# Optimization experiments

Measured on AMD Instinct MI355X. Metric: run time of the kernel, lower is better.

## Reference

```python
import jax, jax.numpy as jnp
import numpy as np

N = 100000
E = 1600000
D_IN, H1, H2 = 64, 128, 64
ATT = 32


def _mean_aggregate(feat, src, dst, num_nodes):
    # gather source features per edge, scatter-sum to destinations, divide by in-degree
    summed = jax.ops.segment_sum(feat[src], dst, num_segments=num_nodes)  # [N, d]
    deg = jax.ops.segment_sum(jnp.ones((src.shape[0],), feat.dtype), dst, num_segments=num_nodes)
    return summed / jnp.maximum(deg, 1.0)[:, None]


def setup_inputs() -> dict:
    key = jax.random.key(0)
    ks = jax.random.split(key, 16)
    x = jax.random.normal(ks[0], (N, D_IN), dtype=jnp.float32)
    edge_index = jax.random.randint(ks[1], (2, E), 0, N, dtype=jnp.int64)

    def lin(k, fan_in, fan_out):
        bound = 1.0 / np.sqrt(fan_in)
        return jax.random.uniform(k, (fan_in, fan_out), jnp.float32, -bound, bound)

    params = {
        'W1_l': lin(ks[2], D_IN, H1), 'W1_r': lin(ks[3], D_IN, H1),
        'b1': jnp.zeros((H1,), jnp.float32),
        'W2_l': lin(ks[4], H1, H2), 'W2_r': lin(ks[5], H1, H2),
        'b2': jnp.zeros((H2,), jnp.float32),
        'Wa': lin(ks[6], H2, ATT), 'ba': jnp.zeros((ATT,), jnp.float32),
        'ctx': jax.random.normal(ks[7], (ATT,), jnp.float32),
        'Wc1': lin(ks[8], H2, H2 // 2), 'bc1': jnp.zeros((H2 // 2,), jnp.float32),
        'Wc2': lin(ks[9], H2 // 2, 1), 'bc2': jnp.zeros((1,), jnp.float32),
    }
    return {'x': x, 'edge_index': edge_index, **params}


def reference(x, edge_index, W1_l, W1_r, b1, W2_l, W2_r, b2, Wa, ba, ctx, Wc1, bc1, Wc2, bc2):
    src, dst = edge_index[0], edge_index[1]
    ionm_alerts = x[:, -1]  # [N]

    # GraphSAGE layer 1 (mean aggr): lin_l(mean_neighbors) + lin_r(x_self)
    agg1 = _mean_aggregate(x, src, dst, N)
    h = jax.nn.relu(agg1 @ W1_l + b1 + x @ W1_r)  # [N, H1]
    # F.dropout(training=False) -> identity

    # GraphSAGE layer 2
    agg2 = _mean_aggregate(h, src, dst, N)
    h = jax.nn.relu(agg2 @ W2_l + b2 + h @ W2_r)  # [N, H2]

    # attention with IONM alert boost (+0.4)
    scores = jnp.tanh(h @ Wa + ba)            # [N, ATT]
    w = scores @ ctx + ionm_alerts * 0.4       # [N]
    w = jax.nn.softmax(w, axis=0)
    h = h * w[:, None]

    pooled = jnp.mean(h, axis=0, keepdims=True)  # [1, H2]

    # classifier head (Dropout identity in eval)
    z = jax.nn.relu(pooled @ Wc1 + bc1)
    return jax.nn.sigmoid(z @ Wc2 + bc2)  # [1, 1]
```

## Files before the change

kernel.cpp:

```cpp
#include <hip/hip_runtime.h>
#include <math.h>

#define N_NODES 100000
#define E_EDGES 1600000
#define D_IN 64
#define HID1 128
#define HID2 64
#define ATT 32
#define CAP 64
#define AT_STRIDE 136
#define NRANGE 4
#define RNODES (N_NODES / NRANGE)
#define NPART 64
#define XCAST_BLOCKS ((N_NODES * 16 + 255) / 256)
#define SCAT_BLOCKS 1024

typedef unsigned int uint32;
typedef unsigned short ushort;
typedef __attribute__((ext_vector_type(8))) short short8;
typedef __attribute__((ext_vector_type(4))) float float4v;

#define NTL(p) __builtin_nontemporal_load(&(p))

__device__ inline uint32 bf16rn(float f){ uint32 u = __float_as_uint(f); return (u + 0x7fffu + ((u >> 16) & 1u)) >> 16; }
__device__ inline uint32 packbf2(float a, float b){ return bf16rn(a) | (bf16rn(b) << 16); }

#if __has_builtin(__builtin_amdgcn_cvt_f32_fp8) && __has_builtin(__builtin_amdgcn_cvt_pk_fp8_f32)
#define HW_FP8 1
#endif

__device__ inline uint32 fp8_enc_sw(float f){
    float a = fabsf(f);
    uint32 s = (__float_as_uint(f) >> 24) & 0x80u;
    if (!(a >= 0.001953125f)) return s;
    if (a > 448.f) return s | 0x7Eu;
    if (a < 0.015625f){
        uint32 c = (uint32)rintf(a * 512.f);
        return s | c;
    }
    int e; float m = frexpf(a, &e);
    int E = e - 1;
    float mant = 2.f * m;
    uint32 mc = (uint32)rintf((mant - 1.f) * 8.f);
    uint32 Ec = (uint32)(E + 7);
    if (mc == 8u){ mc = 0u; Ec += 1u; }
    if (Ec >= 16u || (Ec == 15u && mc > 6u)) return s | 0x7Eu;
    return s | (Ec << 3) | mc;
}

__device__ inline float fp8_dec_sw(uint32 c){
    uint32 s = (c & 0x80u) << 24;
    uint32 E = (c >> 3) & 0xFu, m = c & 7u;
    float v;
    if (E == 0) v = (float)m * 0.001953125f;
    else v = __uint_as_float(((E + 120u) << 23) | (m << 20));
    return __uint_as_float(__float_as_uint(v) | s);
}

__device__ inline uint32 enc4(float a, float b, float c, float d){
#ifdef HW_FP8
    int r = __builtin_amdgcn_cvt_pk_fp8_f32(a, b, 0, false);
    r = __builtin_amdgcn_cvt_pk_fp8_f32(c, d, r, true);
    return (uint32)r;
#else
    return fp8_enc_sw(a) | (fp8_enc_sw(b) << 8) | (fp8_enc_sw(c) << 16) | (fp8_enc_sw(d) << 24);
#endif
}

__device__ inline void dec4acc(uint32 w, float& a0, float& a1, float& a2, float& a3){
#ifdef HW_FP8
    a0 += __builtin_amdgcn_cvt_f32_fp8((int)w, 0);
    a1 += __builtin_amdgcn_cvt_f32_fp8((int)w, 1);
    a2 += __builtin_amdgcn_cvt_f32_fp8((int)w, 2);
    a3 += __builtin_amdgcn_cvt_f32_fp8((int)w, 3);
#else
    a0 += fp8_dec_sw(w & 0xffu);
    a1 += fp8_dec_sw((w >> 8) & 0xffu);
    a2 += fp8_dec_sw((w >> 16) & 0xffu);
    a3 += fp8_dec_sw(w >> 24);
#endif
}

__global__ void k_mega(const float* __restrict__ x,
                       const int* __restrict__ src, const int* __restrict__ dst,
                       const float* __restrict__ W1l, const float* __restrict__ W1r,
                       const float* __restrict__ W2l, const float* __restrict__ W2r,
                       uint32* __restrict__ xb, uint32* __restrict__ xq,
                       uint32* __restrict__ vq,
                       ushort* __restrict__ wt1g, ushort* __restrict__ wt2g,
                       int* __restrict__ cnt, int* __restrict__ ssrc){
    int b = blockIdx.x, t = threadIdx.x;
    if (b < XCAST_BLOCKS){
        int i = b * 256 + t;
        if (i < N_NODES * 16){
            float4v v = NTL(((const float4v*)x)[i]);
            xb[2 * i]     = packbf2(v.x, v.y);
            xb[2 * i + 1] = packbf2(v.z, v.w);
            xq[i] = enc4(v.x, v.y, v.z, v.w);
        }
        return;
    }
    if (b < XCAST_BLOCKS + 2){
        int sub = b - XCAST_BLOCKS;
        ushort* dstp = (sub == 0) ? wt1g : wt2g;
        for (int idx = t; idx < 128 * 128; idx += 256){
            int nn = idx >> 7, kk = idx & 127;
            float v;
            if (sub == 0) v = (kk < 64) ? W1l[kk * 128 + nn] : W1r[(kk - 64) * 128 + nn];
            else          v = (nn < 64) ? W2l[kk * 64 + nn]  : W2r[kk * 64 + (nn - 64)];
            dstp[nn * 128 + kk] = (ushort)bf16rn(v);
        }
        if (sub == 0){
            if (t < 16) xq[(size_t)N_NODES * 16 + t] = 0u;
            else if (t < 32) vq[(size_t)N_NODES * 16 + (t - 16)] = 0u;
        }
        return;
    }
    int rel = b - (XCAST_BLOCKS + 2);
    int range = rel & (NRANGE - 1);
    int blk   = rel >> 2;
    int lo = range * RNODES, hi = lo + RNODES;
    int stride = (SCAT_BLOCKS >> 2) * 256;
    for (int i = blk * 256 + t; i < E_EDGES; i += stride){
        int d = NTL(dst[i]);
        if (d >= lo && d < hi){
            int pos = atomicAdd(&cnt[d], 1);
            if (pos < CAP) ssrc[d * CAP + pos] = NTL(src[i]);
        }
    }
}

__device__ inline void gather8_fp8(const uint32* __restrict__ tab,
                                   const int* __restrict__ ssrc,
                                   const int* __restrict__ cnt,
                                   int n0, int lane,
                                   float acc[8][4], int cct[8]){
    int q = lane >> 4, p = lane & 15;
    int nn = n0 + (lane & 7);
    int ccl_ = cnt[nn];
    int cc[8];
    #pragma unroll
    for (int j = 0; j < 8; j++){
        int c = __shfl(ccl_, j, 64);
        cct[j] = c;
        cc[j] = min(c, CAP);
    }
    #pragma unroll
    for (int j = 0; j < 8; j++){ acc[j][0] = acc[j][1] = acc[j][2] = acc[j][3] = 0.f; }
    int cmax = 0;
    #pragma unroll
    for (int j = 0; j < 8; j++) cmax = max(cmax, cc[j]);
    if (cmax == 0) return;
    int se[8];
    #pragma unroll
    for (int j = 0; j < 8; j++){
        se[j] = (lane < cc[j]) ? NTL(ssrc[(n0 + j) * CAP + lane]) : N_NODES;
    }
    int iters = (cmax + 3) >> 2;
    uint32 w[8];
    #pragma unroll
    for (int j = 0; j < 8; j++){
        int s = __shfl(se[j], q, 64);
        w[j] = tab[(uint32)s * 16u + p];
    }
    for (int it = 0; it < iters; it++){
        uint32 wn[8];
        bool more = (it + 1 < iters);
        int idxn = (it + 1) * 4 + q;
        if (more){
            #pragma unroll
            for (int j = 0; j < 8; j++){
                int s = __shfl(se[j], idxn, 64);
                wn[j] = tab[(uint32)s * 16u + p];
            }
        }
        #pragma unroll
        for (int j = 0; j < 8; j++)
            dec4acc(w[j], acc[j][0], acc[j][1], acc[j][2], acc[j][3]);
        if (more){
            #pragma unroll
            for (int j = 0; j < 8; j++) w[j] = wn[j];
        }
    }
    #pragma unroll
    for (int j = 0; j < 8; j++){
        acc[j][0] += __shfl_xor(acc[j][0], 16, 64); acc[j][1] += __shfl_xor(acc[j][1], 16, 64);
        acc[j][2] += __shfl_xor(acc[j][2], 16, 64); acc[j][3] += __shfl_xor(acc[j][3], 16, 64);
        acc[j][0] += __shfl_xor(acc[j][0], 32, 64); acc[j][1] += __shfl_xor(acc[j][1], 32, 64);
        acc[j][2] += __shfl_xor(acc[j][2], 32, 64); acc[j][3] += __shfl_xor(acc[j][3], 32, 64);
    }
}

__global__ __launch_bounds__(256) void k_layer1(
    const uint32* __restrict__ xq, const uint32* __restrict__ xb,
    const int* __restrict__ ssrc, const int* __restrict__ cnt,
    const ushort* __restrict__ wt1g, const ushort* __restrict__ wt2g,
    const float* __restrict__ b1, const float* __restrict__ b2,
    uint32* __restrict__ vq, float* __restrict__ r2f){
    __shared__ ushort smem[2 * 32 * AT_STRIDE];
    ushort* at  = smem;
    ushort* at2 = smem + 32 * AT_STRIDE;
    float* vstage = (float*)smem;
    int t = threadIdx.x, wave = t >> 6, lane = t & 63;
    int nb0 = blockIdx.x * 32;
    int n0 = nb0 + wave * 8;

    int m0 = t >> 3, ch = t & 7;
    uint4 xval = *(const uint4*)&xb[(size_t)(nb0 + m0) * 32 + ch * 4];

    float acc[8][4]; int cct[8];
    gather8_fp8(xq, ssrc, cnt, n0, lane, acc, cct);
    int p = lane & 15;
    if (lane < 16){
        #pragma unroll
        for (int j = 0; j < 8; j++){
            float inv = 1.f / fmaxf((float)cct[j], 1.f);
            uint2 o;
            o.x = packbf2(acc[j][0] * inv, acc[j][1] * inv);
            o.y = packbf2(acc[j][2] * inv, acc[j][3] * inv);
            *(uint2*)&at[(wave * 8 + j) * AT_STRIDE + 4 * p] = o;
        }
    }
    *(uint4*)((uint32*)(at + m0 * AT_STRIDE + 64) + ch * 4) = xval;
    __syncthreads();

    int cidx = lane & 15, quad = lane >> 4;
    int mt = wave >> 1;
    int nbase = (wave & 1) * 64;
    float4v c[4];
    #pragma unroll
    for (int nt = 0; nt < 4; nt++) c[nt] = (float4v){0.f,0.f,0.f,0.f};
    #pragma unroll
    for (int kt = 0; kt < 4; kt++){
        short8 a = *(short8*)(at + ((mt * 16 + cidx) * AT_STRIDE + kt * 32 + quad * 8));
        #pragma unroll
        for (int nt = 0; nt < 4; nt++){
            short8 b = *(const short8*)(wt1g + ((nbase + nt * 16 + cidx) * 128 + kt * 32 + quad * 8));
            c[nt] = __builtin_amdgcn_mfma_f32_16x16x32_bf16(a, b, c[nt], 0, 0, 0);
        }
    }
    #pragma unroll
    for (int nt = 0; nt < 4; nt++){
        float bb = b1[nbase + nt * 16 + cidx];
        #pragma unroll
        for (int i = 0; i < 4; i++){
            int row = quad * 4 + i;
            at2[(mt * 16 + row) * AT_STRIDE + nbase + nt * 16 + cidx] =
                (ushort)bf16rn(fmaxf(c[nt][i] + bb, 0.f));
        }
    }
    __syncthreads();
    #pragma unroll
    for (int nt = 0; nt < 4; nt++) c[nt] = (float4v){0.f,0.f,0.f,0.f};
    #pragma unroll
    for (int kt = 0; kt < 4; kt++){
        short8 a = *(short8*)(at2 + ((mt * 16 + cidx) * AT_STRIDE + kt * 32 + quad * 8));
        #pragma unroll
        for (int nt = 0; nt < 4; nt++){
            short8 b = *(const short8*)(wt2g + ((nbase + nt * 16 + cidx) * 128 + kt * 32 + quad * 8));
            c[nt] = __builtin_amdgcn_mfma_f32_16x16x32_bf16(a, b, c[nt], 0, 0, 0);
        }
    }
    if (nbase == 0){
        #pragma unroll
        for (int nt = 0; nt < 4; nt++){
            #pragma unroll
            for (int i = 0; i < 4; i++){
                int row = quad * 4 + i;
                vstage[(mt * 16 + row) * 65 + nt * 16 + cidx] = c[nt][i];
            }
        }
    } else {
        #pragma unroll
        for (int nt = 0; nt < 4; nt++){
            float bb = b2[nt * 16 + cidx];
            #pragma unroll
            for (int i = 0; i < 4; i++){
                int row = quad * 4 + i;
                size_t node = nb0 + mt * 16 + row;
                r2f[node * 64 + nt * 16 + cidx] = c[nt][i] + bb;
            }
        }
    }
    __syncthreads();
    {
        int m = t >> 3, u = t & 7;
        float f0 = vstage[m * 65 + 8 * u],     f1 = vstage[m * 65 + 8 * u + 1];
        float f2 = vstage[m * 65 + 8 * u + 2], f3 = vstage[m * 65 + 8 * u + 3];
        float f4 = vstage[m * 65 + 8 * u + 4], f5 = vstage[m * 65 + 8 * u + 5];
        float f6 = vstage[m * 65 + 8 * u + 6], f7 = vstage[m * 65 + 8 * u + 7];
        vq[(size_t)(nb0 + m) * 16 + 2 * u]     = enc4(f0, f1, f2, f3);
        vq[(size_t)(nb0 + m) * 16 + 2 * u + 1] = enc4(f4, f5, f6, f7);
    }
}

__global__ __launch_bounds__(256) void k_gather2f(
    const float* __restrict__ x, const uint32* __restrict__ vq,
    const int* __restrict__ ssrc, const int* __restrict__ cnt,
    const float* __restrict__ r2f,
    const float* __restrict__ Wa, const float* __restrict__ ba, const float* __restrict__ ctx,
    float* __restrict__ pooledP, float* __restrict__ Zpart){
    __shared__ float sh2[32][68];
    __shared__ float sew[32];
    __shared__ float sp[4][64];
    int t = threadIdx.x, wave = t >> 6, lane = t & 63;
    int bn0 = blockIdx.x * 32;
    int n0 = bn0 + wave * 8;
    float acc[8][4]; int cct[8];
    gather8_fp8(vq, ssrc, cnt, n0, lane, acc, cct);
    int p = lane & 15;
    if (lane < 16){
        #pragma unroll
        for (int j = 0; j < 8; j++){
            size_t nj = n0 + j;
            float inv = 1.f / fmaxf((float)cct[j], 1.f);
            float4v rr = NTL(*(const float4v*)&r2f[nj * 64 + 4 * p]);
            float4v hv;
            hv.x = fmaxf(acc[j][0] * inv + rr.x, 0.f);
            hv.y = fmaxf(acc[j][1] * inv + rr.y, 0.f);
            hv.z = fmaxf(acc[j][2] * inv + rr.z, 0.f);
            hv.w = fmaxf(acc[j][3] * inv + rr.w, 0.f);
            *(float4v*)&sh2[wave * 8 + j][4 * p] = hv;
        }
    }
    __syncthreads();
    int node = t >> 3;
    int c0 = (t & 7) * 4;
    float s0 = ba[c0], s1 = ba[c0 + 1], s2 = ba[c0 + 2], s3 = ba[c0 + 3];
    #pragma unroll 8
    for (int j = 0; j < 64; j++){
        float hv = sh2[node][j];
        s0 += hv * Wa[j * ATT + c0];
        s1 += hv * Wa[j * ATT + c0 + 1];
        s2 += hv * Wa[j * ATT + c0 + 2];
        s3 += hv * Wa[j * ATT + c0 + 3];
    }
    float pa = tanhf(s0) * ctx[c0] + tanhf(s1) * ctx[c0 + 1]
             + tanhf(s2) * ctx[c0 + 2] + tanhf(s3) * ctx[c0 + 3];
    #pragma unroll
    for (int off = 4; off >= 1; off >>= 1) pa += __shfl_down(pa, off, 8);
    if ((t & 7) == 0){
        int n = bn0 + node;
        float w = pa + NTL(x[(size_t)n * 64 + 63]) * 0.4f;
        sew[node] = expf(w);
    }
    __syncthreads();
    int j = t & 63, q = t >> 6;
    float p4 = 0.f;
    #pragma unroll
    for (int m = 0; m < 8; m++) p4 += sh2[q * 8 + m][j] * sew[q * 8 + m];
    sp[q][j] = p4;
    __syncthreads();
    if (t < 64){
        float s = sp[0][t] + sp[1][t] + sp[2][t] + sp[3][t];
        atomicAdd(&pooledP[(blockIdx.x & (NPART - 1)) * 64 + t], s);
    }
    if (t == 64){
        float z = 0.f;
        #pragma unroll
        for (int m = 0; m < 32; m++) z += sew[m];
        atomicAdd(&Zpart[blockIdx.x & (NPART - 1)], z);
    }
}

__global__ void k_final(const float* __restrict__ pooledP, const float* __restrict__ Zpart,
                        const float* __restrict__ Wc1, const float* __restrict__ bc1,
                        const float* __restrict__ Wc2, const float* __restrict__ bc2,
                        float* __restrict__ out){
    __shared__ float sp[64], sz[32];
    __shared__ float Zs;
    int t = threadIdx.x;
    float s = 0.f;
    for (int q = 0; q < NPART; q++) s += pooledP[q * 64 + t];
    if (t == 0){
        float z = 0.f;
        for (int q = 0; q < NPART; q++) z += Zpart[q];
        Zs = z;
    }
    __syncthreads();
    float scale = 1.0f / (Zs * (float)N_NODES);
    sp[t] = s * scale;
    __syncthreads();
    if (t < 32){
        float a = bc1[t];
        #pragma unroll 8
        for (int j = 0; j < 64; j++) a += sp[j] * Wc1[j * 32 + t];
        sz[t] = fmaxf(a, 0.f);
    }
    __syncthreads();
    if (t == 0){
        float a = bc2[0];
        #pragma unroll
        for (int i = 0; i < 32; i++) a += sz[i] * Wc2[i];
        out[0] = 1.0f / (1.0f + expf(-a));
    }
}

extern "C" void kernel_launch(void* const* d_in, const int* in_sizes, int n_in,
                              void* d_out, int out_size, void* d_ws, size_t ws_size,
                              hipStream_t stream) {
    const float* x   = (const float*)d_in[0];
    const int*   ei  = (const int*)d_in[1];
    const int*   src = ei;
    const int*   dst = ei + E_EDGES;
    const float* W1l = (const float*)d_in[2];
    const float* W1r = (const float*)d_in[3];
    const float* b1  = (const float*)d_in[4];
    const float* W2l = (const float*)d_in[5];
    const float* W2r = (const float*)d_in[6];
    const float* b2  = (const float*)d_in[7];
    const float* Wa  = (const float*)d_in[8];
    const float* ba  = (const float*)d_in[9];
    const float* ctx = (const float*)d_in[10];
    const float* Wc1 = (const float*)d_in[11];
    const float* bc1 = (const float*)d_in[12];
    const float* Wc2 = (const float*)d_in[13];
    const float* bc2 = (const float*)d_in[14];

    char* p = (char*)d_ws;
    int* cnt    = (int*)p;                 p += (size_t)N_NODES * 4;
    int* ssrc   = (int*)p;                 p += (size_t)N_NODES * CAP * 4;
    uint32* xb  = (uint32*)p;              p += (size_t)N_NODES * 32 * 4;
    uint32* xq  = (uint32*)p;              p += (size_t)(N_NODES + 1) * 16 * 4;
    uint32* vq  = (uint32*)p;              p += (size_t)(N_NODES + 1) * 16 * 4;
    float* r2f  = (float*)p;               p += (size_t)N_NODES * 64 * 4;
    ushort* wt1g = (ushort*)p;             p += 128 * 128 * 2;
    ushort* wt2g = (ushort*)p;             p += 128 * 128 * 2;
    float* pooledP = (float*)p;            p += NPART * 64 * 4;
    float* Zpart   = (float*)p;            p += NPART * 4;

    hipMemsetAsync(cnt, 0, (size_t)N_NODES * 4, stream);
    hipMemsetAsync(pooledP, 0, (NPART * 64 + NPART) * 4, stream);

    k_mega<<<XCAST_BLOCKS + 2 + SCAT_BLOCKS, 256, 0, stream>>>(
        x, src, dst, W1l, W1r, W2l, W2r, xb, xq, vq, wt1g, wt2g, cnt, ssrc);

    k_layer1<<<(N_NODES + 31) / 32, 256, 0, stream>>>(xq, xb, ssrc, cnt,
                                                      wt1g, wt2g, b1, b2, vq, r2f);
    k_gather2f<<<(N_NODES + 31) / 32, 256, 0, stream>>>(x, vq, ssrc, cnt, r2f,
                                                        Wa, ba, ctx, pooledP, Zpart);
    k_final<<<1, 64, 0, stream>>>(pooledP, Zpart, Wc1, bc1, Wc2, bc2, (float*)d_out);
}
```

Baseline: 341.9 us.

## Deepen gather prefetch, split edge scatter into more node ranges, drop memset

The fp8 neighbor gather now prefetches two iterations ahead with double-buffered registers instead of one, giving more memory-level parallelism for the random table loads. The edge bucketing scatter splits destinations into 16 node ranges instead of 4, with an interleaved range mapping, so each block's atomics and ssrc writes touch a smaller address window. In exchange each block scans a larger share of the edge list. The separate memset of the pooled partial buffers is removed and block 0 of layer1 zeroes them instead, saving one launch.

```diff
diff --git a/kernel.cpp b/kernel.cpp
--- a/kernel.cpp
+++ b/kernel.cpp
@@ -9,7 +9,7 @@
 #define ATT 32
 #define CAP 64
 #define AT_STRIDE 136
-#define NRANGE 4
+#define NRANGE 16
 #define RNODES (N_NODES / NRANGE)
 #define NPART 64
 #define XCAST_BLOCKS ((N_NODES * 16 + 255) / 256)
@@ -117,10 +117,10 @@
         return;
     }
     int rel = b - (XCAST_BLOCKS + 2);
-    int range = rel & (NRANGE - 1);
-    int blk   = rel >> 2;
+    int range = ((rel & 7) << 1) | ((rel >> 3) & 1);
+    int blk   = rel >> 4;
     int lo = range * RNODES, hi = lo + RNODES;
-    int stride = (SCAT_BLOCKS >> 2) * 256;
+    int stride = (SCAT_BLOCKS >> 4) * 256;
     for (int i = blk * 256 + t; i < E_EDGES; i += stride){
         int d = NTL(dst[i]);
         if (d >= lo && d < hi){
@@ -153,33 +153,41 @@
     if (cmax == 0) return;
     int se[8];
     #pragma unroll
-    for (int j = 0; j < 8; j++){
+    for (int j = 0; j < 8; j++)
         se[j] = (lane < cc[j]) ? NTL(ssrc[(n0 + j) * CAP + lane]) : N_NODES;
-    }
     int iters = (cmax + 3) >> 2;
-    uint32 w[8];
+    uint32 w0[8], w1[8];
     #pragma unroll
     for (int j = 0; j < 8; j++){
         int s = __shfl(se[j], q, 64);
-        w[j] = tab[(uint32)s * 16u + p];
+        w0[j] = tab[(uint32)s * 16u + p];
+    }
+    if (iters > 1){
+        #pragma unroll
+        for (int j = 0; j < 8; j++){
+            int s = __shfl(se[j], 4 + q, 64);
+            w1[j] = tab[(uint32)s * 16u + p];
+        }
     }
     for (int it = 0; it < iters; it++){
         uint32 wn[8];
-        bool more = (it + 1 < iters);
-        int idxn = (it + 1) * 4 + q;
-        if (more){
+        bool more2 = (it + 2 < iters);
+        if (more2){
+            int idx = (it + 2) * 4 + q;
             #pragma unroll
             for (int j = 0; j < 8; j++){
-                int s = __shfl(se[j], idxn, 64);
+                int s = __shfl(se[j], idx, 64);
                 wn[j] = tab[(uint32)s * 16u + p];
             }
         }
         #pragma unroll
         for (int j = 0; j < 8; j++)
-            dec4acc(w[j], acc[j][0], acc[j][1], acc[j][2], acc[j][3]);
-        if (more){
+            dec4acc(w0[j], acc[j][0], acc[j][1], acc[j][2], acc[j][3]);
+        #pragma unroll
+        for (int j = 0; j < 8; j++) w0[j] = w1[j];
+        if (more2){
             #pragma unroll
-            for (int j = 0; j < 8; j++) w[j] = wn[j];
+            for (int j = 0; j < 8; j++) w1[j] = wn[j];
         }
     }
     #pragma unroll
@@ -196,12 +204,16 @@
     const int* __restrict__ ssrc, const int* __restrict__ cnt,
     const ushort* __restrict__ wt1g, const ushort* __restrict__ wt2g,
     const float* __restrict__ b1, const float* __restrict__ b2,
-    uint32* __restrict__ vq, float* __restrict__ r2f){
+    uint32* __restrict__ vq, float* __restrict__ r2f,
+    float* __restrict__ pzero){
     __shared__ ushort smem[2 * 32 * AT_STRIDE];
     ushort* at  = smem;
     ushort* at2 = smem + 32 * AT_STRIDE;
     float* vstage = (float*)smem;
     int t = threadIdx.x, wave = t >> 6, lane = t & 63;
+    if (blockIdx.x == 0){
+        for (int i = t; i < NPART * 65; i += 256) pzero[i] = 0.f;
+    }
     int nb0 = blockIdx.x * 32;
     int n0 = nb0 + wave * 8;
 
@@ -430,13 +442,12 @@
     float* Zpart   = (float*)p;            p += NPART * 4;
 
     hipMemsetAsync(cnt, 0, (size_t)N_NODES * 4, stream);
-    hipMemsetAsync(pooledP, 0, (NPART * 64 + NPART) * 4, stream);
 
     k_mega<<<XCAST_BLOCKS + 2 + SCAT_BLOCKS, 256, 0, stream>>>(
         x, src, dst, W1l, W1r, W2l, W2r, xb, xq, vq, wt1g, wt2g, cnt, ssrc);
 
     k_layer1<<<(N_NODES + 31) / 32, 256, 0, stream>>>(xq, xb, ssrc, cnt,
-                                                      wt1g, wt2g, b1, b2, vq, r2f);
+                                                      wt1g, wt2g, b1, b2, vq, r2f, pooledP);
     k_gather2f<<<(N_NODES + 31) / 32, 256, 0, stream>>>(x, vq, ssrc, cnt, r2f,
                                                         Wa, ba, ctx, pooledP, Zpart);
     k_final<<<1, 64, 0, stream>>>(pooledP, Zpart, Wc1, bc1, Wc2, bc2, (float*)d_out);
```

After: 411.5 us. 20.3% more time.
